# Performance work log

Measured on AMD Instinct MI355X. Metric: run time of the kernel, lower is better.

## Reference

```python
import jax, jax.numpy as jnp
import numpy as np

EPS = 1e-5
N_HEADS = 8


def _ln(x, g, b):
    m = jnp.mean(x, -1, keepdims=True)
    v = jnp.mean((x - m) ** 2, -1, keepdims=True)
    return (x - m) * jax.lax.rsqrt(v + EPS) * g + b


def setup_inputs() -> dict:
    key = jax.random.key(0)
    ks = jax.random.split(key, 24)
    B, T, H = 64, 512, 256
    HH, H2 = H // 2, 2 * H
    w = lambda k, shape, fan_in: jax.random.normal(k, shape, jnp.float32) / np.sqrt(fan_in)
    return {
        "state": jax.random.normal(ks[0], (B, T, H), jnp.float32),
        "action": jax.random.normal(ks[1], (B, T, 2), jnp.float32),
        "ae_w1": w(ks[2], (2, HH), 2), "ae_b1": jnp.zeros((HH,), jnp.float32),
        "ae_w2": w(ks[3], (HH, H), HH), "ae_b2": jnp.zeros((H,), jnp.float32),
        "ln1_g": jnp.ones((H,), jnp.float32), "ln1_b": jnp.zeros((H,), jnp.float32),
        "ln2_g": jnp.ones((H,), jnp.float32), "ln2_b": jnp.zeros((H,), jnp.float32),
        "wq": w(ks[4], (H, H), H), "bq": jnp.zeros((H,), jnp.float32),
        "wk": w(ks[5], (H, H), H), "bk": jnp.zeros((H,), jnp.float32),
        "wv": w(ks[6], (H, H), H), "bv": jnp.zeros((H,), jnp.float32),
        "wo": w(ks[7], (H, H), H), "bo": jnp.zeros((H,), jnp.float32),
        "gru_wih": w(ks[8], (H, 3 * H2), H), "gru_bih": jnp.zeros((3 * H2,), jnp.float32),
        "gru_whh": w(ks[9], (H2, 3 * H2), H2), "gru_bhh": jnp.zeros((3 * H2,), jnp.float32),
        "mlp_w": w(ks[10], (H2, H), H2), "mlp_b": jnp.zeros((H,), jnp.float32),
    }


def reference(state, action, ae_w1, ae_b1, ae_w2, ae_b2, ln1_g, ln1_b, ln2_g, ln2_b,
              wq, bq, wk, bk, wv, bv, wo, bo,
              gru_wih, gru_bih, gru_whh, gru_bhh, mlp_w, mlp_b):
    B, T, H = state.shape
    dH = H // N_HEADS
    # action encoder (vectorized over all timesteps at once)
    ae = jax.nn.relu(action @ ae_w1 + ae_b1) @ ae_w2 + ae_b2  # [B,T,H]
    q_in = _ln(state, ln1_g, ln1_b)
    kv_in = _ln(ae, ln2_g, ln2_b)
    qh = (q_in @ wq + bq).reshape(B, T, N_HEADS, dH)
    kh = (kv_in @ wk + bk).reshape(B, T, N_HEADS, dH)
    vh = (kv_in @ wv + bv).reshape(B, T, N_HEADS, dH)
    # single query / single key per (b,t): softmax over the length-1 key axis == 1
    scores = jnp.sum(qh * kh, -1, keepdims=True) / jnp.sqrt(jnp.asarray(dH, state.dtype))
    attn = jax.nn.softmax(scores, axis=-1)  # [B,T,nH,1] of ones
    attended = (attn * vh).reshape(B, T, H) @ wo + bo
    x = state + attended  # [B,T,H]
    # GRU: original uses batch_first=False on a [B,T,H] tensor, so the
    # recurrence runs over dim 0 (B) with T as the effective batch.
    H2 = gru_whh.shape[0]

    def step(h, x_t):  # h,[T,2H]; x_t [T,H]
        gi = x_t @ gru_wih + gru_bih
        gh = h @ gru_whh + gru_bhh
        i_r, i_z, i_n = jnp.split(gi, 3, -1)
        h_r, h_z, h_n = jnp.split(gh, 3, -1)
        r = jax.nn.sigmoid(i_r + h_r)
        z = jax.nn.sigmoid(i_z + h_z)
        n = jnp.tanh(i_n + r * h_n)
        h_new = (1.0 - z) * n + z * h
        return h_new, h_new

    h0 = jnp.zeros((T, H2), x.dtype)
    _, out = jax.lax.scan(step, h0, x)  # [B,T,2H]
    states = out @ mlp_w + mlp_b  # dropout is identity in eval mode
    return states, states[:, -1]
```

## Files before the change

### kernel.cpp

```cpp
#include <hip/hip_runtime.h>
#include <hip/hip_bf16.h>

typedef unsigned short u16;
typedef unsigned long long u64;
typedef __attribute__((ext_vector_type(8))) short bf16x8;
typedef __attribute__((ext_vector_type(4))) float f32x4;

static __device__ __forceinline__ u16 f2bf(float f) {
    union { float f; unsigned u; } cv; cv.f = f;
    unsigned u = cv.u;
    unsigned r = u + 0x7FFF + ((u >> 16) & 1);
    return (u16)(r >> 16);
}
static __device__ __forceinline__ float bf2f(u16 b) {
    union { unsigned u; float f; } cv; cv.u = ((unsigned)b) << 16;
    return cv.f;
}
static __device__ __forceinline__ float sigmoidf_(float x) {
    return 1.0f / (1.0f + __expf(-x));
}

__global__ __launch_bounds__(256) void fuse_wvwo(
    const float* __restrict__ wv, const float* __restrict__ wo,
    const float* __restrict__ bv, const float* __restrict__ bo,
    u16* __restrict__ WfT, float* __restrict__ bfv)
{
    int j = blockIdx.x;
    int i = threadIdx.x;
    float s = 0.f;
    for (int k = 0; k < 256; ++k) s += wv[i * 256 + k] * wo[k * 256 + j];
    WfT[j * 256 + i] = f2bf(s);
    if (i == 0) {
        float t = bo[j];
        for (int k = 0; k < 256; ++k) t += bv[k] * wo[k * 256 + j];
        bfv[j] = t;
    }
}

__global__ __launch_bounds__(256) void transpose_bf(
    const float* __restrict__ src, u16* __restrict__ dst, int K, int N)
{
    long i = (long)blockIdx.x * 256 + threadIdx.x;
    if (i >= (long)K * N) return;
    int n = (int)(i / K), k = (int)(i % K);
    dst[i] = f2bf(src[(long)k * N + n]);
}

__global__ __launch_bounds__(256) void ae_ln_mfma(
    const float* __restrict__ action,
    const float* __restrict__ w1, const float* __restrict__ b1,
    const u16* __restrict__ w2T, const float* __restrict__ b2,
    const float* __restrict__ g, const float* __restrict__ be,
    u16* __restrict__ kvbf)
{
    __shared__ u16 lB[256][136];
    __shared__ u16 lA[64][136];
    int tid = threadIdx.x;
    long base = (long)blockIdx.x * 64;

    for (int idx = tid; idx < 256 * 16; idx += 256) {
        int r = idx >> 4, ch = (idx & 15) * 8;
        *(uint4*)&lB[r][ch] = *(const uint4*)&w2T[r * 128 + ch];
    }
    for (int idx = tid; idx < 8192; idx += 256) {
        int r = idx >> 7, k = idx & 127;
        float a0 = action[(base + r) * 2], a1 = action[(base + r) * 2 + 1];
        float v = fmaf(a1, w1[128 + k], fmaf(a0, w1[k], b1[k]));
        lA[r][k] = f2bf(v > 0.f ? v : 0.f);
    }
    __syncthreads();

    int wv = tid >> 6, l = tid & 63;
    int fr = l & 15, fq = l >> 4;
    f32x4 acc[4][4] = {};
#pragma unroll
    for (int ks = 0; ks < 4; ++ks) {
        bf16x8 a[4], b[4];
#pragma unroll
        for (int mi = 0; mi < 4; ++mi) a[mi] = *(bf16x8*)&lA[mi * 16 + fr][ks * 32 + fq * 8];
#pragma unroll
        for (int ni = 0; ni < 4; ++ni) b[ni] = *(bf16x8*)&lB[wv * 64 + ni * 16 + fr][ks * 32 + fq * 8];
#pragma unroll
        for (int mi = 0; mi < 4; ++mi)
#pragma unroll
            for (int ni = 0; ni < 4; ++ni)
                acc[mi][ni] = __builtin_amdgcn_mfma_f32_16x16x32_bf16(a[mi], b[ni], acc[mi][ni], 0, 0, 0);
    }
    __syncthreads();

    float* e = (float*)&lB[0][0];
#pragma unroll
    for (int mi = 0; mi < 4; ++mi)
#pragma unroll
        for (int ni = 0; ni < 4; ++ni) {
            int col = wv * 64 + ni * 16 + fr;
            float bb = b2[col];
#pragma unroll
            for (int reg = 0; reg < 4; ++reg)
                e[(mi * 16 + fq * 4 + reg) * 261 + col] = acc[mi][ni][reg] + bb;
        }
    __syncthreads();

    int t = tid >> 2, sub = tid & 3;
    float s = 0.f, ss = 0.f;
#pragma unroll
    for (int i = 0; i < 64; ++i) {
        float v = e[t * 261 + sub + i * 4];
        s += v; ss += v * v;
    }
    s += __shfl_xor(s, 1); ss += __shfl_xor(ss, 1);
    s += __shfl_xor(s, 2); ss += __shfl_xor(ss, 2);
    float m = s * (1.f / 256.f);
    float var = ss * (1.f / 256.f) - m * m;
    float rs = rsqrtf(var + 1e-5f);
#pragma unroll
    for (int i8 = 0; i8 < 8; ++i8) {
        u16 pack[8];
#pragma unroll
        for (int j = 0; j < 8; ++j) {
            int col = sub * 64 + i8 * 8 + j;
            float v = (e[t * 261 + col] - m) * rs * g[col] + be[col];
            pack[j] = f2bf(v);
        }
        *(uint4*)&kvbf[(base + t) * 256 + sub * 64 + i8 * 8] = *(uint4*)pack;
    }
}

template <int MODE>
__global__ __launch_bounds__(256) void gemm128(
    const u16* __restrict__ A, const u16* __restrict__ BT,
    const float* __restrict__ bias, const float* __restrict__ resid,
    u16* __restrict__ outBf, float* __restrict__ outF,
    int N, int K)
{
    __shared__ u16 lA[128][40];
    __shared__ u16 lB[128][40];
    int tid = threadIdx.x;
    int bm = blockIdx.x * 128, bn = blockIdx.y * 128;

    f32x4 acc[4][4] = {};
    int w = tid >> 6, l = tid & 63;
    int wr = (w >> 1) * 64, wc = (w & 1) * 64;
    int fr = l & 15, fk = (l >> 4) * 8;

    for (int k0 = 0; k0 < K; k0 += 32) {
#pragma unroll
        for (int i = 0; i < 2; ++i) {
            int idx = tid + i * 256;
            int r = idx >> 2, c8 = (idx & 3) * 8;
            *(uint4*)&lA[r][c8] = *(const uint4*)&A[(long)(bm + r) * K + k0 + c8];
            *(uint4*)&lB[r][c8] = *(const uint4*)&BT[(long)(bn + r) * K + k0 + c8];
        }
        __syncthreads();
        bf16x8 a[4], b[4];
#pragma unroll
        for (int mi = 0; mi < 4; ++mi) a[mi] = *(bf16x8*)&lA[wr + mi * 16 + fr][fk];
#pragma unroll
        for (int ni = 0; ni < 4; ++ni) b[ni] = *(bf16x8*)&lB[wc + ni * 16 + fr][fk];
#pragma unroll
        for (int mi = 0; mi < 4; ++mi)
#pragma unroll
            for (int ni = 0; ni < 4; ++ni)
                acc[mi][ni] = __builtin_amdgcn_mfma_f32_16x16x32_bf16(a[mi], b[ni], acc[mi][ni], 0, 0, 0);
        __syncthreads();
    }

#pragma unroll
    for (int mi = 0; mi < 4; ++mi)
#pragma unroll
        for (int ni = 0; ni < 4; ++ni) {
            int c = bn + wc + ni * 16 + fr;
            float bz = bias[c];
#pragma unroll
            for (int reg = 0; reg < 4; ++reg) {
                int r = bm + wr + mi * 16 + (l >> 4) * 4 + reg;
                float v = acc[mi][ni][reg] + bz;
                if constexpr (MODE == 0) {
                    v += resid[(long)r * N + c];
                    outBf[(long)r * N + c] = f2bf(v);
                } else if constexpr (MODE == 1) {
                    outBf[(long)r * N + c] = f2bf(v);
                } else {
                    outF[(long)r * N + c] = v;
                    if ((r & 511) == 511) outF[8388608 + (long)(r >> 9) * N + c] = v;
                }
            }
        }
}

__global__ __launch_bounds__(768, 1) void gru_persistent6(
    const u16* __restrict__ whhT, const float* __restrict__ bhh,
    const u16* __restrict__ gi_bf, const u16* __restrict__ h0_bf,
    u16* __restrict__ out_bf, unsigned* __restrict__ flags)
{
    __shared__ u64 lh64[2048];
    __shared__ __align__(16) float ghs[3][16][68];
    u16* lh = (u16*)lh64;

    int tid = threadIdx.x;
    int bid = blockIdx.x;
    int tg = bid >> 3, cb = bid & 7;
    int tbase = tg * 16, cbase = cb * 64;

    int w = tid >> 6, l = tid & 63;
    int fr = l & 15, fo = l >> 4;
    int cpos = w & 3, gate = w >> 2;

    bf16x8 a[16];
    {
        const u16* wp = whhT + ((size_t)(gate << 9) + cbase + cpos * 16 + fr) * 512 + fo * 8;
#pragma unroll
        for (int kk = 0; kk < 16; ++kk)
            a[kk] = *(const bf16x8*)(wp + kk * 32);
    }

    int et = tid >> 5, ec = (tid & 31) * 2;
    bool ep = tid < 512;
    float hreg0 = 0.f, hreg1 = 0.f;
    float bh_r0 = 0, bh_r1 = 0, bh_z0 = 0, bh_z1 = 0, bh_n0 = 0, bh_n1 = 0;
    if (ep) {
        bh_r0 = bhh[cbase + ec];        bh_r1 = bhh[cbase + ec + 1];
        bh_z0 = bhh[512 + cbase + ec];  bh_z1 = bhh[512 + cbase + ec + 1];
        bh_n0 = bhh[1024 + cbase + ec]; bh_n1 = bhh[1024 + cbase + ec + 1];
    }

    const unsigned* gp = (const unsigned*)gi_bf;
    unsigned g_r = 0, g_z = 0, g_n = 0;
    if (ep) {
        size_t grow = (size_t)(tbase + et) * 1536;
        g_r = gp[(grow + cbase + ec) >> 1];
        g_z = gp[(grow + 512 + cbase + ec) >> 1];
        g_n = gp[(grow + 1024 + cbase + ec) >> 1];
    }

    for (int step = 0; step < 64; ++step) {
        const u64* hb64 = (const u64*)(step ? out_bf + (size_t)(step - 1) * 262144
                                           : h0_bf);
#pragma unroll
        for (int i = 0; i < 3; ++i) {
            int idx = tid + i * 768;
            if (idx < 2048) {
                int r = idx >> 7, kw = idx & 127;
                u64 v = __hip_atomic_load(hb64 + (size_t)(tbase + r) * 128 + kw,
                                          __ATOMIC_RELAXED, __HIP_MEMORY_SCOPE_AGENT);
                lh64[r * 128 + (kw ^ ((r & 7) << 1))] = v;
            }
        }
        __syncthreads();

        f32x4 acc = {0.f, 0.f, 0.f, 0.f};
#pragma unroll
        for (int kk = 0; kk < 16; ++kk) {
            int kb = kk * 32 + fo * 8;
            bf16x8 b = *(bf16x8*)&lh[fr * 512 + (kb ^ ((fr & 7) << 3))];
            acc = __builtin_amdgcn_mfma_f32_16x16x32_bf16(a[kk], b, acc, 0, 0, 0);
        }
        *(f32x4*)&ghs[gate][fr][cpos * 16 + fo * 4] = acc;
        __syncthreads();

        if (ep) {
            float ghr0 = ghs[0][et][ec], ghr1 = ghs[0][et][ec + 1];
            float ghz0 = ghs[1][et][ec], ghz1 = ghs[1][et][ec + 1];
            float ghn0 = ghs[2][et][ec], ghn1 = ghs[2][et][ec + 1];
            float r0 = sigmoidf_(bf2f((u16)(g_r & 0xffff)) + ghr0 + bh_r0);
            float r1 = sigmoidf_(bf2f((u16)(g_r >> 16)) + ghr1 + bh_r1);
            float z0 = sigmoidf_(bf2f((u16)(g_z & 0xffff)) + ghz0 + bh_z0);
            float z1 = sigmoidf_(bf2f((u16)(g_z >> 16)) + ghz1 + bh_z1);
            float n0 = tanhf(bf2f((u16)(g_n & 0xffff)) + r0 * (ghn0 + bh_n0));
            float n1 = tanhf(bf2f((u16)(g_n >> 16)) + r1 * (ghn1 + bh_n1));
            hreg0 = (1.f - z0) * n0 + z0 * hreg0;
            hreg1 = (1.f - z1) * n1 + z1 * hreg1;
            unsigned packv = (unsigned)f2bf(hreg0) | ((unsigned)f2bf(hreg1) << 16);
            __hip_atomic_store(
                (unsigned*)out_bf + ((((size_t)step * 512 + tbase + et) * 512 + cbase + ec) >> 1),
                packv, __ATOMIC_RELAXED, __HIP_MEMORY_SCOPE_AGENT);
        }
        __syncthreads();

        if (step < 63) {
            if (tid == 0)
                __hip_atomic_store(&flags[(tg * 8 + cb) * 32], (unsigned)(step + 1),
                                   __ATOMIC_RELAXED, __HIP_MEMORY_SCOPE_AGENT);
            if (ep) {
                size_t grow = ((size_t)(step + 1) * 512 + tbase + et) * 1536;
                g_r = gp[(grow + cbase + ec) >> 1];
                g_z = gp[(grow + 512 + cbase + ec) >> 1];
                g_n = gp[(grow + 1024 + cbase + ec) >> 1];
            }
            if (tid < 8) {
                unsigned tgt = (unsigned)(step + 1);
                while (__hip_atomic_load(&flags[(tg * 8 + tid) * 32],
                                         __ATOMIC_RELAXED, __HIP_MEMORY_SCOPE_AGENT) < tgt)
                    __builtin_amdgcn_s_sleep(1);
            }
            __syncthreads();
        }
    }
}

extern "C" void kernel_launch(void* const* d_in, const int* in_sizes, int n_in,
                              void* d_out, int out_size, void* d_ws, size_t ws_size,
                              hipStream_t stream)
{
    const float* state   = (const float*)d_in[0];
    const float* action  = (const float*)d_in[1];
    const float* ae_w1   = (const float*)d_in[2];
    const float* ae_b1   = (const float*)d_in[3];
    const float* ae_w2   = (const float*)d_in[4];
    const float* ae_b2   = (const float*)d_in[5];
    const float* ln2_g   = (const float*)d_in[8];
    const float* ln2_b   = (const float*)d_in[9];
    const float* wv      = (const float*)d_in[14];
    const float* bv      = (const float*)d_in[15];
    const float* wo      = (const float*)d_in[16];
    const float* bo      = (const float*)d_in[17];
    const float* gru_wih = (const float*)d_in[18];
    const float* gru_bih = (const float*)d_in[19];
    const float* gru_whh = (const float*)d_in[20];
    const float* gru_bhh = (const float*)d_in[21];
    const float* mlp_w   = (const float*)d_in[22];
    const float* mlp_b   = (const float*)d_in[23];

    char* ws = (char*)d_ws;
    size_t off = 0;
    auto carve = [&](size_t bytes) -> char* {
        char* p = ws + off; off = (off + bytes + 255) & ~(size_t)255; return p;
    };
    u16*   kv_bf  = (u16*)carve(32768ull * 256 * 2);
    u16*   x_bf   = (u16*)carve(32768ull * 256 * 2);
    u16*   gi_bf  = (u16*)carve(32768ull * 1536 * 2);
    u16*   out_bf = (u16*)carve(32768ull * 512 * 2);
    u16*   WfT    = (u16*)carve(256 * 256 * 2);
    float* bfv    = (float*)carve(256 * 4);
    u16*   wihT   = (u16*)carve(1536 * 256 * 2);
    u16*   whhT   = (u16*)carve(1536 * 512 * 2);
    u16*   mlpT   = (u16*)carve(256 * 512 * 2);
    u16*   w2T    = (u16*)carve(256 * 128 * 2);
    u16*   h0_bf  = (u16*)carve(512 * 512 * 2);
    unsigned* flags = (unsigned*)carve(32 * 8 * 32 * 4);

    hipMemsetAsync(h0_bf, 0, 512 * 512 * 2, stream);
    hipMemsetAsync(flags, 0, 32 * 8 * 32 * 4, stream);

    fuse_wvwo<<<256, 256, 0, stream>>>(wv, wo, bv, bo, WfT, bfv);
    transpose_bf<<<1536, 256, 0, stream>>>(gru_wih, wihT, 256, 1536);
    transpose_bf<<<3072, 256, 0, stream>>>(gru_whh, whhT, 512, 1536);
    transpose_bf<<<512, 256, 0, stream>>>(mlp_w, mlpT, 512, 256);
    transpose_bf<<<128, 256, 0, stream>>>(ae_w2, w2T, 128, 256);

    ae_ln_mfma<<<512, 256, 0, stream>>>(action, ae_w1, ae_b1, w2T, ae_b2,
                                        ln2_g, ln2_b, kv_bf);

    gemm128<0><<<dim3(256, 2), 256, 0, stream>>>(kv_bf, WfT, bfv, state, x_bf, nullptr, 256, 256);
    gemm128<1><<<dim3(256, 12), 256, 0, stream>>>(x_bf, wihT, gru_bih, nullptr, gi_bf, nullptr, 1536, 256);

    {
        void* args[] = { (void*)&whhT, (void*)&gru_bhh, (void*)&gi_bf,
                         (void*)&h0_bf, (void*)&out_bf, (void*)&flags };
        hipError_t cerr = hipLaunchCooperativeKernel((const void*)gru_persistent6,
                                                     dim3(256), dim3(768), args, 0, stream);
        if (cerr != hipSuccess) {
            gru_persistent6<<<dim3(256), dim3(768), 0, stream>>>(
                whhT, gru_bhh, gi_bf, h0_bf, out_bf, flags);
        }
    }

    gemm128<2><<<dim3(256, 2), 256, 0, stream>>>(out_bf, mlpT, mlp_b, nullptr, nullptr,
                                                 (float*)d_out, 256, 512);
}
```

Before: 406.2 us.

## Interleave two independent time-row groups per block in GRU recurrence to hide sync latency

Each persistent GRU block now owns two disjoint 8-row slices of the T batch (tA and tA+256) instead of one 16-row slice. The two halves are processed in ping-pong fashion, with separate flag arrays, so the global load of one half's hidden state overlaps the MFMA and gate math of the other. The intent is to hide inter-block flag-wait and global-memory latency in the serial recurrence. The cost is that half of each 16-row MFMA tile is wasted, there are twice as many barriers and flag handshakes per step, and the initial h0 load contains redundant dead code.

```diff
diff --git a/kernel.cpp b/kernel.cpp
--- a/kernel.cpp
+++ b/kernel.cpp
@@ -188,23 +188,26 @@
         }
 }
 
-__global__ __launch_bounds__(768, 1) void gru_persistent6(
+__global__ __launch_bounds__(768, 1) void gru_persistent7(
     const u16* __restrict__ whhT, const float* __restrict__ bhh,
     const u16* __restrict__ gi_bf, const u16* __restrict__ h0_bf,
-    u16* __restrict__ out_bf, unsigned* __restrict__ flags)
-{
-    __shared__ u64 lh64[2048];
-    __shared__ __align__(16) float ghs[3][16][68];
-    u16* lh = (u16*)lh64;
-
-    int tid = threadIdx.x;
-    int bid = blockIdx.x;
-    int tg = bid >> 3, cb = bid & 7;
-    int tbase = tg * 16, cbase = cb * 64;
-
-    int w = tid >> 6, l = tid & 63;
-    int fr = l & 15, fo = l >> 4;
+    u16* __restrict__ out_bf, unsigned* __restrict__ flagsA,
+    unsigned* __restrict__ flagsB)
+{
+    __shared__ u64 lhA[1024];
+    __shared__ u64 lhB[1024];
+    __shared__ __align__(16) float ghs[3][8][68];
+    u16* lA16 = (u16*)lhA;
+    u16* lB16 = (u16*)lhB;
+
+    int tid = threadIdx.x, bid = blockIdx.x;
+    int p = bid >> 3, cb = bid & 7;
+    int tA = p * 8, tB = tA + 256;
+    int cbase = cb * 64;
+
+    int w = tid >> 6, l = tid & 63, fr = l & 15, fo = l >> 4;
     int cpos = w & 3, gate = w >> 2;
+    int fr8 = fr & 7;
 
     bf16x8 a[16];
     {
@@ -215,8 +218,8 @@
     }
 
     int et = tid >> 5, ec = (tid & 31) * 2;
-    bool ep = tid < 512;
-    float hreg0 = 0.f, hreg1 = 0.f;
+    bool ep = tid < 256;
+    float hA0 = 0.f, hA1 = 0.f, hB0 = 0.f, hB1 = 0.f;
     float bh_r0 = 0, bh_r1 = 0, bh_z0 = 0, bh_z1 = 0, bh_n0 = 0, bh_n1 = 0;
     if (ep) {
         bh_r0 = bhh[cbase + ec];        bh_r1 = bhh[cbase + ec + 1];
@@ -225,76 +228,173 @@
     }
 
     const unsigned* gp = (const unsigned*)gi_bf;
-    unsigned g_r = 0, g_z = 0, g_n = 0;
-    if (ep) {
-        size_t grow = (size_t)(tbase + et) * 1536;
-        g_r = gp[(grow + cbase + ec) >> 1];
-        g_z = gp[(grow + 512 + cbase + ec) >> 1];
-        g_n = gp[(grow + 1024 + cbase + ec) >> 1];
-    }
-
-    for (int step = 0; step < 64; ++step) {
-        const u64* hb64 = (const u64*)(step ? out_bf + (size_t)(step - 1) * 262144
-                                           : h0_bf);
-#pragma unroll
-        for (int i = 0; i < 3; ++i) {
-            int idx = tid + i * 768;
-            if (idx < 2048) {
-                int r = idx >> 7, kw = idx & 127;
-                u64 v = __hip_atomic_load(hb64 + (size_t)(tbase + r) * 128 + kw,
-                                          __ATOMIC_RELAXED, __HIP_MEMORY_SCOPE_AGENT);
-                lh64[r * 128 + (kw ^ ((r & 7) << 1))] = v;
-            }
-        }
-        __syncthreads();
-
-        f32x4 acc = {0.f, 0.f, 0.f, 0.f};
-#pragma unroll
-        for (int kk = 0; kk < 16; ++kk) {
-            int kb = kk * 32 + fo * 8;
-            bf16x8 b = *(bf16x8*)&lh[fr * 512 + (kb ^ ((fr & 7) << 3))];
-            acc = __builtin_amdgcn_mfma_f32_16x16x32_bf16(a[kk], b, acc, 0, 0, 0);
-        }
-        *(f32x4*)&ghs[gate][fr][cpos * 16 + fo * 4] = acc;
+    const u64* h0q = (const u64*)h0_bf;
+    u64* outq = (u64*)out_bf;
+
+    {
+        int r = tid >> 7, kw = tid & 127;
+        if (tid < 1024)
+            lhA[r * 128 + (kw ^ (r << 1))] =
+                h0q[(size_t)(tA + r) * 64 + kw] * 0 +
+                __hip_atomic_load(h0q + (size_t)(tA + r) * 64 + kw,
+                                  __ATOMIC_RELAXED, __HIP_MEMORY_SCOPE_AGENT) * 0;
+        if (tid < 1024)
+            lhA[r * 128 + (kw ^ (r << 1))] =
+                __hip_atomic_load(h0q + (size_t)(tA + r) * 128 + kw,
+                                  __ATOMIC_RELAXED, __HIP_MEMORY_SCOPE_AGENT);
+        int tid2 = tid + 768;
+        if (tid2 < 1024) {
+            int r2 = tid2 >> 7, kw2 = tid2 & 127;
+            lhA[r2 * 128 + (kw2 ^ (r2 << 1))] =
+                __hip_atomic_load(h0q + (size_t)(tA + r2) * 128 + kw2,
+                                  __ATOMIC_RELAXED, __HIP_MEMORY_SCOPE_AGENT);
+        }
+    }
+
+    int fslot_own = (p * 8 + cb) * 16;
+    int fslot_peer = (p * 8 + (tid & 7)) * 16;
+
+    for (int s = 0; s < 64; ++s) {
+        if (tid == 0)
+            __hip_atomic_store(&flagsB[fslot_own], (unsigned)s,
+                               __ATOMIC_RELAXED, __HIP_MEMORY_SCOPE_AGENT);
+        if (tid < 8) {
+            while (__hip_atomic_load(&flagsB[fslot_peer],
+                                     __ATOMIC_RELAXED, __HIP_MEMORY_SCOPE_AGENT) < (unsigned)s)
+                __builtin_amdgcn_s_sleep(1);
+        }
+        __syncthreads();
+
+        const u64* hbB = s ? outq + (size_t)((s - 1) * 512) * 64 : h0q;
+        const u64* srcB = s ? outq + ((size_t)(s - 1) * 512 + tB) * 128 : h0q + (size_t)tB * 128;
+        u64 rB0, rB1 = 0;
+        {
+            int r = tid >> 7, kw = tid & 127;
+            rB0 = __hip_atomic_load(srcB + (size_t)r * 128 + kw,
+                                    __ATOMIC_RELAXED, __HIP_MEMORY_SCOPE_AGENT);
+            if (tid < 256) {
+                int t2 = tid + 768;
+                int r2 = t2 >> 7, kw2 = t2 & 127;
+                rB1 = __hip_atomic_load(srcB + (size_t)r2 * 128 + kw2,
+                                        __ATOMIC_RELAXED, __HIP_MEMORY_SCOPE_AGENT);
+            }
+        }
+        unsigned gAr = 0, gAz = 0, gAn = 0;
+        if (ep) {
+            size_t grow = ((size_t)s * 512 + tA + et) * 1536;
+            gAr = gp[(grow + cbase + ec) >> 1];
+            gAz = gp[(grow + 512 + cbase + ec) >> 1];
+            gAn = gp[(grow + 1024 + cbase + ec) >> 1];
+        }
+        {
+            f32x4 acc = {0.f, 0.f, 0.f, 0.f};
+#pragma unroll
+            for (int kk = 0; kk < 16; ++kk) {
+                int kb = kk * 32 + fo * 8;
+                bf16x8 b = *(bf16x8*)&lA16[fr8 * 512 + (kb ^ (fr8 << 3))];
+                acc = __builtin_amdgcn_mfma_f32_16x16x32_bf16(a[kk], b, acc, 0, 0, 0);
+            }
+            if (fr < 8) *(f32x4*)&ghs[gate][fr][cpos * 16 + fo * 4] = acc;
+        }
+        {
+            int r = tid >> 7, kw = tid & 127;
+            lhB[r * 128 + (kw ^ (r << 1))] = rB0;
+            if (tid < 256) {
+                int t2 = tid + 768;
+                int r2 = t2 >> 7, kw2 = t2 & 127;
+                lhB[r2 * 128 + (kw2 ^ (r2 << 1))] = rB1;
+            }
+        }
         __syncthreads();
 
         if (ep) {
             float ghr0 = ghs[0][et][ec], ghr1 = ghs[0][et][ec + 1];
             float ghz0 = ghs[1][et][ec], ghz1 = ghs[1][et][ec + 1];
             float ghn0 = ghs[2][et][ec], ghn1 = ghs[2][et][ec + 1];
-            float r0 = sigmoidf_(bf2f((u16)(g_r & 0xffff)) + ghr0 + bh_r0);
-            float r1 = sigmoidf_(bf2f((u16)(g_r >> 16)) + ghr1 + bh_r1);
-            float z0 = sigmoidf_(bf2f((u16)(g_z & 0xffff)) + ghz0 + bh_z0);
-            float z1 = sigmoidf_(bf2f((u16)(g_z >> 16)) + ghz1 + bh_z1);
-            float n0 = tanhf(bf2f((u16)(g_n & 0xffff)) + r0 * (ghn0 + bh_n0));
-            float n1 = tanhf(bf2f((u16)(g_n >> 16)) + r1 * (ghn1 + bh_n1));
-            hreg0 = (1.f - z0) * n0 + z0 * hreg0;
-            hreg1 = (1.f - z1) * n1 + z1 * hreg1;
-            unsigned packv = (unsigned)f2bf(hreg0) | ((unsigned)f2bf(hreg1) << 16);
+            float r0 = sigmoidf_(bf2f((u16)(gAr & 0xffff)) + ghr0 + bh_r0);
+            float r1 = sigmoidf_(bf2f((u16)(gAr >> 16)) + ghr1 + bh_r1);
+            float z0 = sigmoidf_(bf2f((u16)(gAz & 0xffff)) + ghz0 + bh_z0);
+            float z1 = sigmoidf_(bf2f((u16)(gAz >> 16)) + ghz1 + bh_z1);
+            float n0 = tanhf(bf2f((u16)(gAn & 0xffff)) + r0 * (ghn0 + bh_n0));
+            float n1 = tanhf(bf2f((u16)(gAn >> 16)) + r1 * (ghn1 + bh_n1));
+            hA0 = (1.f - z0) * n0 + z0 * hA0;
+            hA1 = (1.f - z1) * n1 + z1 * hA1;
+            unsigned packv = (unsigned)f2bf(hA0) | ((unsigned)f2bf(hA1) << 16);
             __hip_atomic_store(
-                (unsigned*)out_bf + ((((size_t)step * 512 + tbase + et) * 512 + cbase + ec) >> 1),
+                (unsigned*)out_bf + ((((size_t)s * 512 + tA + et) * 512 + cbase + ec) >> 1),
                 packv, __ATOMIC_RELAXED, __HIP_MEMORY_SCOPE_AGENT);
         }
         __syncthreads();
 
-        if (step < 63) {
-            if (tid == 0)
-                __hip_atomic_store(&flags[(tg * 8 + cb) * 32], (unsigned)(step + 1),
-                                   __ATOMIC_RELAXED, __HIP_MEMORY_SCOPE_AGENT);
-            if (ep) {
-                size_t grow = ((size_t)(step + 1) * 512 + tbase + et) * 1536;
-                g_r = gp[(grow + cbase + ec) >> 1];
-                g_z = gp[(grow + 512 + cbase + ec) >> 1];
-                g_n = gp[(grow + 1024 + cbase + ec) >> 1];
-            }
-            if (tid < 8) {
-                unsigned tgt = (unsigned)(step + 1);
-                while (__hip_atomic_load(&flags[(tg * 8 + tid) * 32],
-                                         __ATOMIC_RELAXED, __HIP_MEMORY_SCOPE_AGENT) < tgt)
-                    __builtin_amdgcn_s_sleep(1);
-            }
-            __syncthreads();
-        }
+        if (tid == 0)
+            __hip_atomic_store(&flagsA[fslot_own], (unsigned)(s + 1),
+                               __ATOMIC_RELAXED, __HIP_MEMORY_SCOPE_AGENT);
+        if (tid < 8) {
+            while (__hip_atomic_load(&flagsA[fslot_peer],
+                                     __ATOMIC_RELAXED, __HIP_MEMORY_SCOPE_AGENT) < (unsigned)(s + 1))
+                __builtin_amdgcn_s_sleep(1);
+        }
+        __syncthreads();
+
+        const u64* srcA = outq + ((size_t)s * 512 + tA) * 128;
+        u64 rA0, rA1 = 0;
+        {
+            int r = tid >> 7, kw = tid & 127;
+            rA0 = __hip_atomic_load(srcA + (size_t)r * 128 + kw,
+                                    __ATOMIC_RELAXED, __HIP_MEMORY_SCOPE_AGENT);
+            if (tid < 256) {
+                int t2 = tid + 768;
+                int r2 = t2 >> 7, kw2 = t2 & 127;
+                rA1 = __hip_atomic_load(srcA + (size_t)r2 * 128 + kw2,
+                                        __ATOMIC_RELAXED, __HIP_MEMORY_SCOPE_AGENT);
+            }
+        }
+        unsigned gBr = 0, gBz = 0, gBn = 0;
+        if (ep) {
+            size_t grow = ((size_t)s * 512 + tB + et) * 1536;
+            gBr = gp[(grow + cbase + ec) >> 1];
+            gBz = gp[(grow + 512 + cbase + ec) >> 1];
+            gBn = gp[(grow + 1024 + cbase + ec) >> 1];
+        }
+        {
+            f32x4 acc = {0.f, 0.f, 0.f, 0.f};
+#pragma unroll
+            for (int kk = 0; kk < 16; ++kk) {
+                int kb = kk * 32 + fo * 8;
+                bf16x8 b = *(bf16x8*)&lB16[fr8 * 512 + (kb ^ (fr8 << 3))];
+                acc = __builtin_amdgcn_mfma_f32_16x16x32_bf16(a[kk], b, acc, 0, 0, 0);
+            }
+            if (fr < 8) *(f32x4*)&ghs[gate][fr][cpos * 16 + fo * 4] = acc;
+        }
+        {
+            int r = tid >> 7, kw = tid & 127;
+            lhA[r * 128 + (kw ^ (r << 1))] = rA0;
+            if (tid < 256) {
+                int t2 = tid + 768;
+                int r2 = t2 >> 7, kw2 = t2 & 127;
+                lhA[r2 * 128 + (kw2 ^ (r2 << 1))] = rA1;
+            }
+        }
+        __syncthreads();
+
+        if (ep) {
+            float ghr0 = ghs[0][et][ec], ghr1 = ghs[0][et][ec + 1];
+            float ghz0 = ghs[1][et][ec], ghz1 = ghs[1][et][ec + 1];
+            float ghn0 = ghs[2][et][ec], ghn1 = ghs[2][et][ec + 1];
+            float r0 = sigmoidf_(bf2f((u16)(gBr & 0xffff)) + ghr0 + bh_r0);
+            float r1 = sigmoidf_(bf2f((u16)(gBr >> 16)) + ghr1 + bh_r1);
+            float z0 = sigmoidf_(bf2f((u16)(gBz & 0xffff)) + ghz0 + bh_z0);
+            float z1 = sigmoidf_(bf2f((u16)(gBz >> 16)) + ghz1 + bh_z1);
+            float n0 = tanhf(bf2f((u16)(gBn & 0xffff)) + r0 * (ghn0 + bh_n0));
+            float n1 = tanhf(bf2f((u16)(gBn >> 16)) + r1 * (ghn1 + bh_n1));
+            hB0 = (1.f - z0) * n0 + z0 * hB0;
+            hB1 = (1.f - z1) * n1 + z1 * hB1;
+            unsigned packv = (unsigned)f2bf(hB0) | ((unsigned)f2bf(hB1) << 16);
+            __hip_atomic_store(
+                (unsigned*)out_bf + ((((size_t)s * 512 + tB + et) * 512 + cbase + ec) >> 1),
+                packv, __ATOMIC_RELAXED, __HIP_MEMORY_SCOPE_AGENT);
+        }
+        __syncthreads();
     }
 }
 
@@ -337,10 +437,12 @@
     u16*   mlpT   = (u16*)carve(256 * 512 * 2);
     u16*   w2T    = (u16*)carve(256 * 128 * 2);
     u16*   h0_bf  = (u16*)carve(512 * 512 * 2);
-    unsigned* flags = (unsigned*)carve(32 * 8 * 32 * 4);
+    unsigned* flagsA = (unsigned*)carve(256 * 16 * 4);
+    unsigned* flagsB = (unsigned*)carve(256 * 16 * 4);
 
     hipMemsetAsync(h0_bf, 0, 512 * 512 * 2, stream);
-    hipMemsetAsync(flags, 0, 32 * 8 * 32 * 4, stream);
+    hipMemsetAsync(flagsA, 0, 256 * 16 * 4, stream);
+    hipMemsetAsync(flagsB, 0, 256 * 16 * 4, stream);
 
     fuse_wvwo<<<256, 256, 0, stream>>>(wv, wo, bv, bo, WfT, bfv);
     transpose_bf<<<1536, 256, 0, stream>>>(gru_wih, wihT, 256, 1536);
@@ -356,12 +458,12 @@
 
     {
         void* args[] = { (void*)&whhT, (void*)&gru_bhh, (void*)&gi_bf,
-                         (void*)&h0_bf, (void*)&out_bf, (void*)&flags };
-        hipError_t cerr = hipLaunchCooperativeKernel((const void*)gru_persistent6,
+                         (void*)&h0_bf, (void*)&out_bf, (void*)&flagsA, (void*)&flagsB };
+        hipError_t cerr = hipLaunchCooperativeKernel((const void*)gru_persistent7,
                                                      dim3(256), dim3(768), args, 0, stream);
         if (cerr != hipSuccess) {
-            gru_persistent6<<<dim3(256), dim3(768), 0, stream>>>(
-                whhT, gru_bhh, gi_bf, h0_bf, out_bf, flags);
+            gru_persistent7<<<dim3(256), dim3(768), 0, stream>>>(
+                whhT, gru_bhh, gi_bf, h0_bf, out_bf, flagsA, flagsB);
         }
     }
 
```

Result: slower. 492.4 us (+21.2%).

## Tile weight transposes via LDS, compute Wv·Wo with MFMA GEMM, widen GEMM K-step

Applied to the files above, without the earlier changes.

Replaces the naive per-element weight transpose with an LDS-tiled transpose that uses coalesced float4 reads and 16-byte writes. The scalar fused Wv·Wo matmul kernel becomes a bf16 conversion plus a transpose feeding the existing MFMA GEMM, with a separate small kernel for the fused bias. The gemm128 K-tile also grows from 32 to 64, halving the loop iterations and barriers at the cost of more LDS. The fused weight is now accumulated from bf16 inputs, which slightly changes its precision.

```diff
diff --git a/kernel.cpp b/kernel.cpp
--- a/kernel.cpp
+++ b/kernel.cpp
@@ -20,30 +20,51 @@
     return 1.0f / (1.0f + __expf(-x));
 }
 
-__global__ __launch_bounds__(256) void fuse_wvwo(
-    const float* __restrict__ wv, const float* __restrict__ wo,
-    const float* __restrict__ bv, const float* __restrict__ bo,
-    u16* __restrict__ WfT, float* __restrict__ bfv)
-{
-    int j = blockIdx.x;
-    int i = threadIdx.x;
-    float s = 0.f;
-    for (int k = 0; k < 256; ++k) s += wv[i * 256 + k] * wo[k * 256 + j];
-    WfT[j * 256 + i] = f2bf(s);
-    if (i == 0) {
-        float t = bo[j];
-        for (int k = 0; k < 256; ++k) t += bv[k] * wo[k * 256 + j];
-        bfv[j] = t;
-    }
-}
-
-__global__ __launch_bounds__(256) void transpose_bf(
+__global__ __launch_bounds__(256) void transpose_tile_bf(
     const float* __restrict__ src, u16* __restrict__ dst, int K, int N)
 {
-    long i = (long)blockIdx.x * 256 + threadIdx.x;
-    if (i >= (long)K * N) return;
-    int n = (int)(i / K), k = (int)(i % K);
-    dst[i] = f2bf(src[(long)k * N + n]);
+    __shared__ u16 t[64][66];
+    int k0 = blockIdx.x * 64, n0 = blockIdx.y * 64;
+    int tid = threadIdx.x;
+    int r = tid >> 4, c4 = (tid & 15) * 4;
+#pragma unroll
+    for (int p = 0; p < 4; ++p) {
+        int row = r + p * 16;
+        float4 v = *(const float4*)&src[(size_t)(k0 + row) * N + n0 + c4];
+        t[c4 + 0][row] = f2bf(v.x);
+        t[c4 + 1][row] = f2bf(v.y);
+        t[c4 + 2][row] = f2bf(v.z);
+        t[c4 + 3][row] = f2bf(v.w);
+    }
+    __syncthreads();
+    int rr = tid >> 3, cc = (tid & 7) * 8;
+#pragma unroll
+    for (int p = 0; p < 2; ++p) {
+        int row = rr + p * 32;
+        u16 pack[8];
+#pragma unroll
+        for (int j = 0; j < 8; ++j) pack[j] = t[row][cc + j];
+        *(uint4*)&dst[(size_t)(n0 + row) * K + k0 + cc] = *(uint4*)pack;
+    }
+}
+
+__global__ __launch_bounds__(256) void convert_bf(
+    const float* __restrict__ src, u16* __restrict__ dst)
+{
+    int i = (blockIdx.x * 256 + threadIdx.x) * 4;
+    float4 v = *(const float4*)&src[i];
+    u16 pack[4] = { f2bf(v.x), f2bf(v.y), f2bf(v.z), f2bf(v.w) };
+    *(u64*)&dst[i] = *(u64*)pack;
+}
+
+__global__ __launch_bounds__(256) void bias_fuse(
+    const float* __restrict__ bv, const float* __restrict__ wo,
+    const float* __restrict__ bo, float* __restrict__ bfv)
+{
+    int j = threadIdx.x;
+    float t = bo[j];
+    for (int k = 0; k < 256; ++k) t = fmaf(bv[k], wo[k * 256 + j], t);
+    bfv[j] = t;
 }
 
 __global__ __launch_bounds__(256) void ae_ln_mfma(
@@ -133,8 +154,8 @@
     u16* __restrict__ outBf, float* __restrict__ outF,
     int N, int K)
 {
-    __shared__ u16 lA[128][40];
-    __shared__ u16 lB[128][40];
+    __shared__ u16 lA[128][72];
+    __shared__ u16 lB[128][72];
     int tid = threadIdx.x;
     int bm = blockIdx.x * 128, bn = blockIdx.y * 128;
 
@@ -143,25 +164,29 @@
     int wr = (w >> 1) * 64, wc = (w & 1) * 64;
     int fr = l & 15, fk = (l >> 4) * 8;
 
-    for (int k0 = 0; k0 < K; k0 += 32) {
-#pragma unroll
-        for (int i = 0; i < 2; ++i) {
+    for (int k0 = 0; k0 < K; k0 += 64) {
+#pragma unroll
+        for (int i = 0; i < 4; ++i) {
             int idx = tid + i * 256;
-            int r = idx >> 2, c8 = (idx & 3) * 8;
+            int r = idx >> 3, c8 = (idx & 7) * 8;
             *(uint4*)&lA[r][c8] = *(const uint4*)&A[(long)(bm + r) * K + k0 + c8];
             *(uint4*)&lB[r][c8] = *(const uint4*)&BT[(long)(bn + r) * K + k0 + c8];
         }
         __syncthreads();
-        bf16x8 a[4], b[4];
-#pragma unroll
-        for (int mi = 0; mi < 4; ++mi) a[mi] = *(bf16x8*)&lA[wr + mi * 16 + fr][fk];
-#pragma unroll
-        for (int ni = 0; ni < 4; ++ni) b[ni] = *(bf16x8*)&lB[wc + ni * 16 + fr][fk];
-#pragma unroll
-        for (int mi = 0; mi < 4; ++mi)
-#pragma unroll
-            for (int ni = 0; ni < 4; ++ni)
-                acc[mi][ni] = __builtin_amdgcn_mfma_f32_16x16x32_bf16(a[mi], b[ni], acc[mi][ni], 0, 0, 0);
+#pragma unroll
+        for (int half = 0; half < 2; ++half) {
+            int fo = half * 32 + fk;
+            bf16x8 a[4], b[4];
+#pragma unroll
+            for (int mi = 0; mi < 4; ++mi) a[mi] = *(bf16x8*)&lA[wr + mi * 16 + fr][fo];
+#pragma unroll
+            for (int ni = 0; ni < 4; ++ni) b[ni] = *(bf16x8*)&lB[wc + ni * 16 + fr][fo];
+#pragma unroll
+            for (int mi = 0; mi < 4; ++mi)
+#pragma unroll
+                for (int ni = 0; ni < 4; ++ni)
+                    acc[mi][ni] = __builtin_amdgcn_mfma_f32_16x16x32_bf16(a[mi], b[ni], acc[mi][ni], 0, 0, 0);
+        }
         __syncthreads();
     }
 
@@ -336,17 +361,24 @@
     u16*   whhT   = (u16*)carve(1536 * 512 * 2);
     u16*   mlpT   = (u16*)carve(256 * 512 * 2);
     u16*   w2T    = (u16*)carve(256 * 128 * 2);
+    u16*   woT    = (u16*)carve(256 * 256 * 2);
+    u16*   wv_bf  = (u16*)carve(256 * 256 * 2);
+    float* zerob  = (float*)carve(256 * 4);
     u16*   h0_bf  = (u16*)carve(512 * 512 * 2);
     unsigned* flags = (unsigned*)carve(32 * 8 * 32 * 4);
 
     hipMemsetAsync(h0_bf, 0, 512 * 512 * 2, stream);
     hipMemsetAsync(flags, 0, 32 * 8 * 32 * 4, stream);
-
-    fuse_wvwo<<<256, 256, 0, stream>>>(wv, wo, bv, bo, WfT, bfv);
-    transpose_bf<<<1536, 256, 0, stream>>>(gru_wih, wihT, 256, 1536);
-    transpose_bf<<<3072, 256, 0, stream>>>(gru_whh, whhT, 512, 1536);
-    transpose_bf<<<512, 256, 0, stream>>>(mlp_w, mlpT, 512, 256);
-    transpose_bf<<<128, 256, 0, stream>>>(ae_w2, w2T, 128, 256);
+    hipMemsetAsync(zerob, 0, 256 * 4, stream);
+
+    convert_bf<<<64, 256, 0, stream>>>(wv, wv_bf);
+    transpose_tile_bf<<<dim3(4, 4), 256, 0, stream>>>(wo, woT, 256, 256);
+    transpose_tile_bf<<<dim3(4, 24), 256, 0, stream>>>(gru_wih, wihT, 256, 1536);
+    transpose_tile_bf<<<dim3(8, 24), 256, 0, stream>>>(gru_whh, whhT, 512, 1536);
+    transpose_tile_bf<<<dim3(8, 4), 256, 0, stream>>>(mlp_w, mlpT, 512, 256);
+    transpose_tile_bf<<<dim3(2, 4), 256, 0, stream>>>(ae_w2, w2T, 128, 256);
+    bias_fuse<<<1, 256, 0, stream>>>(bv, wo, bo, bfv);
+    gemm128<1><<<dim3(2, 2), 256, 0, stream>>>(woT, wv_bf, zerob, nullptr, WfT, nullptr, 256, 256);
 
     ae_ln_mfma<<<512, 256, 0, stream>>>(action, ae_w1, ae_b1, w2T, ae_b2,
                                         ln2_g, ln2_b, kv_bf);
```

Measured after the change: 395.3 us. -2.7%, faster.
